# Kernel optimization log

Hardware: AMD Instinct MI355X
Metric: run time of the kernel (lower is better)

The kernel has to match this reference:

```python
import jax, jax.numpy as jnp
import numpy as np

H, RANK, BATCH, T = 1024, 4, 128, 256


def setup_inputs() -> dict:
    key = jax.random.key(0)
    ks = jax.random.split(key, 6)
    s = 1.0 / np.sqrt(H)  # glorot-ish scale for params
    return {
        "x": jax.random.normal(ks[0], (BATCH, T, H), jnp.float32),
        "h0": jnp.zeros((BATCH, H), jnp.float32),
        "d": jax.random.normal(ks[1], (H,), jnp.float32) * s,
        "L": jax.random.normal(ks[2], (H, RANK), jnp.float32) * s,
        "R": jax.random.normal(ks[3], (RANK, H), jnp.float32) * s,
        "B": jax.random.normal(ks[4], (H, H), jnp.float32) * s,
    }


def reference(x, h0, d, L, R, B):
    # Input projection B.T @ x_t for all steps at once (one big GEMM):
    # (B.T @ x)_i = sum_j B[j,i] x[j]  ->  x @ B
    xB = jnp.einsum("bth,hk->btk", x, B)  # [batch, T, H]

    def step(h, u):  # h: [batch, H], u: [batch, H]
        # diagonal + rank-4 low-rank update: d*h + L @ (R @ h) + B.T @ x
        low_rank = (h @ R.T) @ L.T  # [batch, H]
        h = jnp.tanh(d * h + low_rank + u)
        return h, h

    _, hs = jax.lax.scan(step, h0, jnp.swapaxes(xB, 0, 1))  # hs: [T, batch, H]
    return jnp.swapaxes(hs, 0, 1)  # [batch, T, H]
```

## Files before the change

kernel.cpp:

```cpp
#include <hip/hip_runtime.h>
#include <hip/hip_bf16.h>

#define H_DIM  1024
#define RANK_  4
#define BATCH_ 128
#define TSTEPS 256
#define M_DIM  (BATCH_ * TSTEPS)

typedef __bf16 bf16x8 __attribute__((ext_vector_type(8)));
typedef float  floatx4 __attribute__((ext_vector_type(4)));
typedef unsigned short ushortx8 __attribute__((ext_vector_type(8)));

__device__ __forceinline__ unsigned short f2bf(float f) {
    unsigned u = __float_as_uint(f);
    u += 0x7FFFu + ((u >> 16) & 1u);
    return (unsigned short)(u >> 16);
}


__global__ __launch_bounds__(256) void cvt_x_kernel(const float* __restrict__ x,
                                                    unsigned short* __restrict__ xb) {
    size_t i = ((size_t)blockIdx.x * 256 + threadIdx.x) * 8;
    float4 v0 = *(const float4*)(x + i);
    float4 v1 = *(const float4*)(x + i + 4);
    ushortx8 o;
    o[0] = f2bf(v0.x); o[1] = f2bf(v0.y); o[2] = f2bf(v0.z); o[3] = f2bf(v0.w);
    o[4] = f2bf(v1.x); o[5] = f2bf(v1.y); o[6] = f2bf(v1.z); o[7] = f2bf(v1.w);
    *(ushortx8*)(xb + i) = o;
}

__global__ __launch_bounds__(256) void cvt_bt_kernel(const float* __restrict__ B,
                                                     unsigned short* __restrict__ Bt) {
    __shared__ float tl[32][33];
    int tx = threadIdx.x & 31, ty = threadIdx.x >> 5;
    int k0 = blockIdx.y * 32, n0 = blockIdx.x * 32;
#pragma unroll
    for (int j = 0; j < 4; ++j)
        tl[ty + 8 * j][tx] = B[(size_t)(k0 + ty + 8 * j) * H_DIM + n0 + tx];
    __syncthreads();
#pragma unroll
    for (int j = 0; j < 4; ++j)
        Bt[(size_t)(n0 + ty + 8 * j) * H_DIM + k0 + tx] = f2bf(tl[tx][ty + 8 * j]);
}


#define TM 128
#define TN 128
#define BK 64
#define BKP 72

__global__ __launch_bounds__(256) void gemm_bf16_kernel(const unsigned short* __restrict__ A,
                                                        const unsigned short* __restrict__ Bt,
                                                        float* __restrict__ C) {
    __shared__ unsigned short As[TM * BKP];
    __shared__ unsigned short Bs[TN * BKP];

    const int tid  = threadIdx.x;
    const int lane = tid & 63;
    const int wid  = tid >> 6;
    const int wm = (wid >> 1) * 64, wn = (wid & 1) * 64;
    const int bm = blockIdx.x >> 3, bn = blockIdx.x & 7;
    const int m0 = bm * TM, n0 = bn * TN;

    const int sr = tid >> 3;
    const int sc = (tid & 7) * 8;
    const unsigned short* Ag = A  + (size_t)(m0 + sr) * H_DIM + sc;
    const unsigned short* Bg = Bt + (size_t)(n0 + sr) * H_DIM + sc;

    floatx4 acc[4][4];
#pragma unroll
    for (int i = 0; i < 4; ++i)
#pragma unroll
        for (int j = 0; j < 4; ++j) acc[i][j] = (floatx4){0.f, 0.f, 0.f, 0.f};

    const int fr = lane & 15;
    const int fk = (lane >> 4) * 8;

    for (int kt = 0; kt < H_DIM; kt += BK) {
        ushortx8 ar[4], br[4];
#pragma unroll
        for (int p = 0; p < 4; ++p) {
            ar[p] = *(const ushortx8*)(Ag + (size_t)(32 * p) * H_DIM + kt);
            br[p] = *(const ushortx8*)(Bg + (size_t)(32 * p) * H_DIM + kt);
        }
        __syncthreads();
#pragma unroll
        for (int p = 0; p < 4; ++p) {
            *(ushortx8*)(As + (sr + 32 * p) * BKP + sc) = ar[p];
            *(ushortx8*)(Bs + (sr + 32 * p) * BKP + sc) = br[p];
        }
        __syncthreads();
#pragma unroll
        for (int ks = 0; ks < BK; ks += 32) {
            bf16x8 af[4], bfr[4];
#pragma unroll
            for (int i = 0; i < 4; ++i)
                af[i] = *(const bf16x8*)(As + (wm + i * 16 + fr) * BKP + ks + fk);
#pragma unroll
            for (int j = 0; j < 4; ++j)
                bfr[j] = *(const bf16x8*)(Bs + (wn + j * 16 + fr) * BKP + ks + fk);
#pragma unroll
            for (int i = 0; i < 4; ++i)
#pragma unroll
                for (int j = 0; j < 4; ++j)
                    acc[i][j] = __builtin_amdgcn_mfma_f32_16x16x32_bf16(af[i], bfr[j], acc[i][j], 0, 0, 0);
        }
    }

    const int cr = (lane >> 4) * 4;
    const int cc = lane & 15;
#pragma unroll
    for (int i = 0; i < 4; ++i)
#pragma unroll
        for (int j = 0; j < 4; ++j) {
            size_t base = (size_t)(m0 + wm + i * 16 + cr) * H_DIM + (n0 + wn + j * 16 + cc);
#pragma unroll
            for (int r = 0; r < 4; ++r)
                C[base + (size_t)r * H_DIM] = acc[i][j][r];
        }
}

__global__ __launch_bounds__(256) void gemm_fp32_fallback(const float* __restrict__ A,
                                                          const float* __restrict__ B,
                                                          float* __restrict__ C) {
    __shared__ float As[64][20];
    __shared__ float Bs[16][68];
    const int tid = threadIdx.x;
    const int bm = blockIdx.x >> 4, bn = blockIdx.x & 15;
    const int m0 = bm * 64, n0 = bn * 64;
    const int tx = (tid & 15) * 4, ty = (tid >> 4) * 4;
    float acc[4][4];
#pragma unroll
    for (int i = 0; i < 4; ++i)
#pragma unroll
        for (int j = 0; j < 4; ++j) acc[i][j] = 0.f;

    for (int kk = 0; kk < H_DIM; kk += 16) {
        float4 av = *(const float4*)(A + (size_t)(m0 + (tid >> 2)) * H_DIM + kk + (tid & 3) * 4);
        float4 bv = *(const float4*)(B + (size_t)(kk + (tid >> 4)) * H_DIM + n0 + (tid & 15) * 4);
        __syncthreads();
        *(float4*)&As[tid >> 2][(tid & 3) * 4] = av;
        *(float4*)&Bs[tid >> 4][(tid & 15) * 4] = bv;
        __syncthreads();
#pragma unroll
        for (int k = 0; k < 16; ++k) {
            float a_[4], b_[4];
#pragma unroll
            for (int i = 0; i < 4; ++i) a_[i] = As[ty + i][k];
#pragma unroll
            for (int j = 0; j < 4; ++j) b_[j] = Bs[k][tx + j];
#pragma unroll
            for (int i = 0; i < 4; ++i)
#pragma unroll
                for (int j = 0; j < 4; ++j) acc[i][j] += a_[i] * b_[j];
        }
    }
#pragma unroll
    for (int i = 0; i < 4; ++i)
#pragma unroll
        for (int j = 0; j < 4; ++j)
            C[(size_t)(m0 + ty + i) * H_DIM + n0 + tx + j] = acc[i][j];
}


__device__ __forceinline__ float tanh_fast(float x) {
    float ax = fabsf(x);
    float e  = __expf(-2.0f * ax);
    float t  = (1.0f - e) * __builtin_amdgcn_rcpf(1.0f + e);
    return copysignf(t, x);
}

__global__ __launch_bounds__(256) void scan_kernel(const float* __restrict__ h0,
                                                   const float* __restrict__ d,
                                                   const float* __restrict__ Lm,
                                                   const float* __restrict__ Rm,
                                                   float* __restrict__ io) {
    const int b = blockIdx.x, tid = threadIdx.x;
    const int lane = tid & 63, wv = tid >> 6;
    const int e = tid * 4;

    float4 dv4 = *(const float4*)(d + e);
    float dd[4] = {dv4.x, dv4.y, dv4.z, dv4.w};
    float4 hv4 = *(const float4*)(h0 + (size_t)b * H_DIM + e);
    float h[4] = {hv4.x, hv4.y, hv4.z, hv4.w};

    float Lv[4][4], Rv[4][4];
#pragma unroll
    for (int i = 0; i < 4; ++i) {
        float4 t = *(const float4*)(Lm + (size_t)(e + i) * RANK_);
        Lv[i][0] = t.x; Lv[i][1] = t.y; Lv[i][2] = t.z; Lv[i][3] = t.w;
    }
#pragma unroll
    for (int j = 0; j < 4; ++j) {
        float4 t = *(const float4*)(Rm + (size_t)j * H_DIM + e);
        Rv[j][0] = t.x; Rv[j][1] = t.y; Rv[j][2] = t.z; Rv[j][3] = t.w;
    }

    float* iob = io + (size_t)b * TSTEPS * H_DIM + e;
    __shared__ float red[2][4][4];

    float4 u0 = *(const float4*)(iob);
    float4 u1 = *(const float4*)(iob + H_DIM);

    for (int t = 0; t < TSTEPS; ++t) {
        float4 u = u0;
        u0 = u1;
        if (t + 2 < TSTEPS) u1 = *(const float4*)(iob + (size_t)(t + 2) * H_DIM);

        float pr[4];
#pragma unroll
        for (int j = 0; j < 4; ++j)
            pr[j] = Rv[j][0] * h[0] + Rv[j][1] * h[1] + Rv[j][2] * h[2] + Rv[j][3] * h[3];
#pragma unroll
        for (int s = 32; s > 0; s >>= 1) {
#pragma unroll
            for (int j = 0; j < 4; ++j) pr[j] += __shfl_xor(pr[j], s, 64);
        }
        if (lane == 0) {
            float4 w = {pr[0], pr[1], pr[2], pr[3]};
            *(float4*)&red[t & 1][wv][0] = w;
        }
        __syncthreads();
        float4 r0 = *(const float4*)&red[t & 1][0][0];
        float4 r1 = *(const float4*)&red[t & 1][1][0];
        float4 r2 = *(const float4*)&red[t & 1][2][0];
        float4 r3 = *(const float4*)&red[t & 1][3][0];
        float r[4] = {r0.x + r1.x + r2.x + r3.x, r0.y + r1.y + r2.y + r3.y,
                      r0.z + r1.z + r2.z + r3.z, r0.w + r1.w + r2.w + r3.w};

        float uu[4] = {u.x, u.y, u.z, u.w};
#pragma unroll
        for (int i = 0; i < 4; ++i) {
            float a = dd[i] * h[i] + uu[i];
            a += Lv[i][0] * r[0] + Lv[i][1] * r[1] + Lv[i][2] * r[2] + Lv[i][3] * r[3];
            h[i] = tanh_fast(a);
        }
        float4 o = {h[0], h[1], h[2], h[3]};
        *(float4*)(iob + (size_t)t * H_DIM) = o;
    }
}


extern "C" void kernel_launch(void* const* d_in, const int* in_sizes, int n_in,
                              void* d_out, int out_size, void* d_ws, size_t ws_size,
                              hipStream_t stream) {
    const float* x  = (const float*)d_in[0];
    const float* h0 = (const float*)d_in[1];
    const float* dd = (const float*)d_in[2];
    const float* L  = (const float*)d_in[3];
    const float* R  = (const float*)d_in[4];
    const float* B  = (const float*)d_in[5];
    float* out = (float*)d_out;

    const size_t need = (size_t)M_DIM * H_DIM * sizeof(unsigned short)
                      + (size_t)H_DIM * H_DIM * sizeof(unsigned short);
    if (ws_size >= need) {
        unsigned short* xb = (unsigned short*)d_ws;
        unsigned short* Bt = xb + (size_t)M_DIM * H_DIM;
        cvt_x_kernel<<<(M_DIM * H_DIM) / (256 * 8), 256, 0, stream>>>(x, xb);
        cvt_bt_kernel<<<dim3(32, 32), 256, 0, stream>>>(B, Bt);
        gemm_bf16_kernel<<<(M_DIM / TM) * (H_DIM / TN), 256, 0, stream>>>(xb, Bt, out);
    } else {
        gemm_fp32_fallback<<<(M_DIM / 64) * (H_DIM / 64), 256, 0, stream>>>(x, B, out);
    }
    scan_kernel<<<BATCH_, 256, 0, stream>>>(h0, dd, L, R, out);
}
```

Before: 466.2 us.

## Use direct global-to-LDS loads in GEMM and DPP reductions with lighter barriers in scan

The GEMM now loads tiles straight from global memory into LDS through global_load_lds, in a fragment-major layout that drops the padding and the register round-trip. The scan kernel replaces shuffle-based wave reductions with DPP row operations and swaps __syncthreads for a barrier that waits only on LDS counters. It also deepens the prefetch of the input projection to four steps. The aim is to shorten the per-step latency of the serial scan and to cut staging overhead in the GEMM. The risks are correctness of the DPP reduction lane pattern, since the result is read from lane 63, and the LDS-only barrier possibly not ordering the global loads as intended.

```diff
diff --git a/kernel.cpp b/kernel.cpp
--- a/kernel.cpp
+++ b/kernel.cpp
@@ -47,13 +47,12 @@
 #define TM 128
 #define TN 128
 #define BK 64
-#define BKP 72
 
 __global__ __launch_bounds__(256) void gemm_bf16_kernel(const unsigned short* __restrict__ A,
                                                         const unsigned short* __restrict__ Bt,
                                                         float* __restrict__ C) {
-    __shared__ unsigned short As[TM * BKP];
-    __shared__ unsigned short Bs[TN * BKP];
+    __shared__ unsigned short As[TM * BK];
+    __shared__ unsigned short Bs[TN * BK];
 
     const int tid  = threadIdx.x;
     const int lane = tid & 63;
@@ -62,10 +61,22 @@
     const int bm = blockIdx.x >> 3, bn = blockIdx.x & 7;
     const int m0 = bm * TM, n0 = bn * TN;
 
-    const int sr = tid >> 3;
-    const int sc = (tid & 7) * 8;
-    const unsigned short* Ag = A  + (size_t)(m0 + sr) * H_DIM + sc;
-    const unsigned short* Bg = Bt + (size_t)(n0 + sr) * H_DIM + sc;
+    const int lr = lane & 15;
+    const int lk = (lane >> 4) * 8;
+
+    const unsigned short* ag[4];
+    const unsigned short* bg[4];
+    unsigned short* asl[4];
+    unsigned short* bsl[4];
+#pragma unroll
+    for (int p = 0; p < 4; ++p) {
+        const int ab = wid * 4 + p;
+        const int rb = ab >> 1, kb = ab & 1;
+        ag[p]  = A  + (size_t)(m0 + rb * 16 + lr) * H_DIM + kb * 32 + lk;
+        bg[p]  = Bt + (size_t)(n0 + rb * 16 + lr) * H_DIM + kb * 32 + lk;
+        asl[p] = As + ab * 512;
+        bsl[p] = Bs + ab * 512;
+    }
 
     floatx4 acc[4][4];
 #pragma unroll
@@ -73,37 +84,36 @@
 #pragma unroll
         for (int j = 0; j < 4; ++j) acc[i][j] = (floatx4){0.f, 0.f, 0.f, 0.f};
 
-    const int fr = lane & 15;
-    const int fk = (lane >> 4) * 8;
-
     for (int kt = 0; kt < H_DIM; kt += BK) {
-        ushortx8 ar[4], br[4];
+        __syncthreads();
 #pragma unroll
         for (int p = 0; p < 4; ++p) {
-            ar[p] = *(const ushortx8*)(Ag + (size_t)(32 * p) * H_DIM + kt);
-            br[p] = *(const ushortx8*)(Bg + (size_t)(32 * p) * H_DIM + kt);
-        }
-        __syncthreads();
-#pragma unroll
-        for (int p = 0; p < 4; ++p) {
-            *(ushortx8*)(As + (sr + 32 * p) * BKP + sc) = ar[p];
-            *(ushortx8*)(Bs + (sr + 32 * p) * BKP + sc) = br[p];
-        }
-        __syncthreads();
-#pragma unroll
-        for (int ks = 0; ks < BK; ks += 32) {
-            bf16x8 af[4], bfr[4];
+            __builtin_amdgcn_global_load_lds(
+                (const __attribute__((address_space(1))) void*)(ag[p] + kt),
+                (__attribute__((address_space(3))) void*)asl[p], 16, 0, 0);
+            __builtin_amdgcn_global_load_lds(
+                (const __attribute__((address_space(1))) void*)(bg[p] + kt),
+                (__attribute__((address_space(3))) void*)bsl[p], 16, 0, 0);
+        }
+        __syncthreads();
+#pragma unroll
+        for (int kb = 0; kb < 2; ++kb) {
+            bf16x8 af[4], bfv[4];
+#pragma unroll
+            for (int i = 0; i < 4; ++i) {
+                const int rbA = (wm >> 4) + i;
+                af[i] = *(const bf16x8*)(As + ((rbA * 2 + kb) << 9) + (lane << 3));
+            }
+#pragma unroll
+            for (int j = 0; j < 4; ++j) {
+                const int rbB = (wn >> 4) + j;
+                bfv[j] = *(const bf16x8*)(Bs + ((rbB * 2 + kb) << 9) + (lane << 3));
+            }
 #pragma unroll
             for (int i = 0; i < 4; ++i)
-                af[i] = *(const bf16x8*)(As + (wm + i * 16 + fr) * BKP + ks + fk);
-#pragma unroll
-            for (int j = 0; j < 4; ++j)
-                bfr[j] = *(const bf16x8*)(Bs + (wn + j * 16 + fr) * BKP + ks + fk);
-#pragma unroll
-            for (int i = 0; i < 4; ++i)
 #pragma unroll
                 for (int j = 0; j < 4; ++j)
-                    acc[i][j] = __builtin_amdgcn_mfma_f32_16x16x32_bf16(af[i], bfr[j], acc[i][j], 0, 0, 0);
+                    acc[i][j] = __builtin_amdgcn_mfma_f32_16x16x32_bf16(af[i], bfv[j], acc[i][j], 0, 0, 0);
         }
     }
 
@@ -170,6 +180,25 @@
     return copysignf(t, x);
 }
 
+__device__ __forceinline__ void barrier_lds_only() {
+    asm volatile("s_waitcnt lgkmcnt(0)\n\ts_barrier" ::: "memory");
+}
+
+template <int CTRL, int RMASK>
+__device__ __forceinline__ float dpp_add(float x) {
+    int v = __builtin_amdgcn_update_dpp(0, __float_as_int(x), CTRL, RMASK, 0xf, true);
+    return x + __int_as_float(v);
+}
+__device__ __forceinline__ float wave_sum64(float x) {
+    x = dpp_add<0x111, 0xf>(x);
+    x = dpp_add<0x112, 0xf>(x);
+    x = dpp_add<0x114, 0xf>(x);
+    x = dpp_add<0x118, 0xf>(x);
+    x = dpp_add<0x142, 0xa>(x);
+    x = dpp_add<0x143, 0xc>(x);
+    return x;
+}
+
 __global__ __launch_bounds__(256) void scan_kernel(const float* __restrict__ h0,
                                                    const float* __restrict__ d,
                                                    const float* __restrict__ Lm,
@@ -199,44 +228,43 @@
     float* iob = io + (size_t)b * TSTEPS * H_DIM + e;
     __shared__ float red[2][4][4];
 
-    float4 u0 = *(const float4*)(iob);
-    float4 u1 = *(const float4*)(iob + H_DIM);
-
-    for (int t = 0; t < TSTEPS; ++t) {
-        float4 u = u0;
-        u0 = u1;
-        if (t + 2 < TSTEPS) u1 = *(const float4*)(iob + (size_t)(t + 2) * H_DIM);
-
-        float pr[4];
-#pragma unroll
-        for (int j = 0; j < 4; ++j)
-            pr[j] = Rv[j][0] * h[0] + Rv[j][1] * h[1] + Rv[j][2] * h[2] + Rv[j][3] * h[3];
-#pragma unroll
-        for (int s = 32; s > 0; s >>= 1) {
-#pragma unroll
-            for (int j = 0; j < 4; ++j) pr[j] += __shfl_xor(pr[j], s, 64);
-        }
-        if (lane == 0) {
-            float4 w = {pr[0], pr[1], pr[2], pr[3]};
-            *(float4*)&red[t & 1][wv][0] = w;
-        }
-        __syncthreads();
-        float4 r0 = *(const float4*)&red[t & 1][0][0];
-        float4 r1 = *(const float4*)&red[t & 1][1][0];
-        float4 r2 = *(const float4*)&red[t & 1][2][0];
-        float4 r3 = *(const float4*)&red[t & 1][3][0];
-        float r[4] = {r0.x + r1.x + r2.x + r3.x, r0.y + r1.y + r2.y + r3.y,
-                      r0.z + r1.z + r2.z + r3.z, r0.w + r1.w + r2.w + r3.w};
-
-        float uu[4] = {u.x, u.y, u.z, u.w};
-#pragma unroll
-        for (int i = 0; i < 4; ++i) {
-            float a = dd[i] * h[i] + uu[i];
-            a += Lv[i][0] * r[0] + Lv[i][1] * r[1] + Lv[i][2] * r[2] + Lv[i][3] * r[3];
-            h[i] = tanh_fast(a);
-        }
-        float4 o = {h[0], h[1], h[2], h[3]};
-        *(float4*)(iob + (size_t)t * H_DIM) = o;
+    float4 u[4];
+#pragma unroll
+    for (int s = 0; s < 4; ++s) u[s] = *(const float4*)(iob + (size_t)s * H_DIM);
+
+    for (int t = 0; t < TSTEPS; t += 4) {
+#pragma unroll
+        for (int s = 0; s < 4; ++s) {
+            const int tt = t + s;
+            float pr[4];
+#pragma unroll
+            for (int j = 0; j < 4; ++j)
+                pr[j] = Rv[j][0] * h[0] + Rv[j][1] * h[1] + Rv[j][2] * h[2] + Rv[j][3] * h[3];
+#pragma unroll
+            for (int j = 0; j < 4; ++j) pr[j] = wave_sum64(pr[j]);
+            if (lane == 63) {
+                float4 w; w.x = pr[0]; w.y = pr[1]; w.z = pr[2]; w.w = pr[3];
+                *(float4*)&red[s & 1][wv][0] = w;
+            }
+            barrier_lds_only();
+            float4 r0 = *(const float4*)&red[s & 1][0][0];
+            float4 r1 = *(const float4*)&red[s & 1][1][0];
+            float4 r2 = *(const float4*)&red[s & 1][2][0];
+            float4 r3 = *(const float4*)&red[s & 1][3][0];
+            float r[4] = {r0.x + r1.x + r2.x + r3.x, r0.y + r1.y + r2.y + r3.y,
+                          r0.z + r1.z + r2.z + r3.z, r0.w + r1.w + r2.w + r3.w};
+
+            float uu[4] = {u[s].x, u[s].y, u[s].z, u[s].w};
+#pragma unroll
+            for (int i = 0; i < 4; ++i) {
+                float a = fmaf(dd[i], h[i], uu[i]);
+                a += Lv[i][0] * r[0] + Lv[i][1] * r[1] + Lv[i][2] * r[2] + Lv[i][3] * r[3];
+                h[i] = tanh_fast(a);
+            }
+            float4 o; o.x = h[0]; o.y = h[1]; o.z = h[2]; o.w = h[3];
+            *(float4*)(iob + (size_t)tt * H_DIM) = o;
+            if (tt + 4 < TSTEPS) u[s] = *(const float4*)(iob + (size_t)(tt + 4) * H_DIM);
+        }
     }
 }
 
```

After: 461.9 us. About the same (-0.9%).
